# Optimization experiments

Hardware: AMD Instinct MI355X
Metric: run time of the kernel (lower is better)

Reference implementation:

```python
import jax, jax.numpy as jnp
from jax import lax
import numpy as np

RF = 1024   # receptive field
MGC = 60    # mgc feature size
UPS = 200   # upsample factor
MIX = 10    # num mixtures
FS = 256    # filter size
F = 2       # mgc frames
N = F * UPS
SQRT_HALF = 0.70710678118


def setup_inputs() -> dict:
    key = jax.random.key(0)
    ks = jax.random.split(key, 30)
    g = lambda i, shape, s=0.05: jax.random.normal(ks[i], shape, dtype=jnp.float32) * s
    return dict(
        signal=g(0, (N + RF,), 0.3),
        mgc=g(1, (F, MGC), 1.0),
        cond_w=g(2, (MGC * UPS, MGC)), cond_b=g(3, (MGC * UPS,)),
        l0_win=g(4, (FS, 1, 2)), l0_bin=g(5, (FS,)),
        l0_wg=g(6, (FS, 1, 2)), l0_bg=g(7, (FS,)),
        l0_wr=g(8, (FS, 1, 2)), l0_br=g(9, (FS,)),
        lw_in=g(10, (9, FS, FS, 2)), lb_in=g(11, (9, FS)),
        lw_g=g(12, (9, FS, FS, 2)), lb_g=g(13, (9, FS)),
        lw_r=g(14, (9, FS, FS, 2)), lb_r=g(15, (9, FS)),
        cw_in=g(16, (10, FS, MGC)), cb_in=g(17, (10, FS)),
        cw_g=g(18, (10, FS, MGC)), cb_g=g(19, (10, FS)),
        pre_w=g(20, (256, FS)), pre_b=g(21, (256,)),
        mean_w=g(22, (MIX, 256)), mean_b=g(23, (MIX,)),
        std_w=g(24, (MIX, 256)), std_b=g(25, (MIX,)),
        logit_w=g(26, (MIX, 256)), logit_b=g(27, (MIX,)),
    )


def _cond_conv(x, cond, win, bin_, wg, bg, wr, br, wci, bci, wcg, bcg):
    # x: [N, Cin, L]; cond: [N, MGC] -> out: [N, FS, L//2]
    conv = lambda w, b: lax.conv_general_dilated(
        x, w, window_strides=(2,), padding='VALID',
        dimension_numbers=('NCH', 'OIH', 'NCH')) + b[None, :, None]
    it = jnp.tanh(conv(win, bin_) + (cond @ wci.T + bci)[:, :, None])
    gt = jax.nn.sigmoid(conv(wg, bg) + (cond @ wcg.T + bcg)[:, :, None])
    return (it * gt + conv(wr, br)) * SQRT_HALF


def _forward(signal, mgc, cond_w, cond_b,
             l0_win, l0_bin, l0_wg, l0_bg, l0_wr, l0_br,
             lw_in, lb_in, lw_g, lb_g, lw_r, lb_r,
             cw_in, cb_in, cw_g, cb_g,
             pre_w, pre_b, mean_w, mean_b, std_w, std_b, logit_w, logit_b):
    n = signal.shape[0] - RF
    # sliding windows: [n, 1, RF]
    idx = jnp.arange(n)[:, None] + jnp.arange(RF)[None, :]
    x = signal[idx][:, None, :]
    # conditioning: [F, MGC] -> [F, MGC*UPS] -> [F*UPS, MGC]
    cond = jnp.tanh(mgc @ cond_w.T + cond_b).reshape(-1, MGC)
    # WaveNet stack: 10 stride-2 gated conv layers, L: 1024 -> 1
    x = _cond_conv(x, cond, l0_win, l0_bin, l0_wg, l0_bg, l0_wr, l0_br,
                   cw_in[0], cb_in[0], cw_g[0], cb_g[0])
    for i in range(9):
        x = _cond_conv(x, cond, lw_in[i], lb_in[i], lw_g[i], lb_g[i],
                       lw_r[i], lb_r[i], cw_in[i + 1], cb_in[i + 1],
                       cw_g[i + 1], cb_g[i + 1])
    pre = jax.nn.relu(x[:, :, 0] @ pre_w.T + pre_b)  # [n, 256]
    mean = pre @ mean_w.T + mean_b
    stdev = pre @ std_w.T + std_b
    logits = pre @ logit_w.T + logit_b
    return mean, stdev, logits


def reference(signal, mgc, cond_w, cond_b,
              l0_win, l0_bin, l0_wg, l0_bg, l0_wr, l0_br,
              lw_in, lb_in, lw_g, lb_g, lw_r, lb_r,
              cw_in, cb_in, cw_g, cb_g,
              pre_w, pre_b, mean_w, mean_b, std_w, std_b, logit_w, logit_b):
    return _forward(signal, mgc, cond_w, cond_b,
                    l0_win, l0_bin, l0_wg, l0_bg, l0_wr, l0_br,
                    lw_in, lb_in, lw_g, lb_g, lw_r, lb_r,
                    cw_in, cb_in, cw_g, cb_g,
                    pre_w, pre_b, mean_w, mean_b, std_w, std_b,
                    logit_w, logit_b)
```

## Files before the change

kernel.cpp:

```cpp
#include <hip/hip_runtime.h>

typedef unsigned short u16;
using bf16x8 = __attribute__((ext_vector_type(8))) short;
using f32x4  = __attribute__((ext_vector_type(4))) float;

#define SQRT_HALF 0.70710678118f

__device__ __forceinline__ u16 f2bf(float f) {
    union { float f; unsigned int i; } x; x.f = f;
    unsigned int i = x.i;
    unsigned int r = (i + 0x7FFFu + ((i >> 16) & 1u)) >> 16;
    return (u16)r;
}
__device__ __forceinline__ float bf2f(u16 u) {
    union { unsigned int i; float f; } x; x.i = ((unsigned int)u) << 16; return x.f;
}
__device__ __forceinline__ float fastrcp(float x) {
    float r; asm("v_rcp_f32 %0, %1" : "=v"(r) : "v"(x)); return r;
}
__device__ __forceinline__ float sigm(float x) {
    return fastrcp(1.0f + __expf(-x));
}
__device__ __forceinline__ float tanh_f(float x) {
    float cx = fminf(fmaxf(x, -12.f), 12.f);
    float e = __expf(2.f * cx);
    return 1.0f - 2.0f * fastrcp(e + 1.0f);
}

__device__ __forceinline__ void gld16(const u16* g, u16* l) {
    __builtin_amdgcn_global_load_lds(
        (const __attribute__((address_space(1))) void*)g,
        (__attribute__((address_space(3))) void*)l,
        16, 0, 0);
}

__global__ __launch_bounds__(256) void xpose_kernel(
        const float* __restrict__ cond_w, const float* __restrict__ cw_in,
        const float* __restrict__ cw_g,
        float* __restrict__ cond_wT, float* __restrict__ cwT_in,
        float* __restrict__ cwT_g) {
    int idx = blockIdx.x * 256 + threadIdx.x;
    if (idx < 720000) {
        int c = idx / 12000, j = idx % 12000;
        cond_wT[idx] = cond_w[(size_t)j * 60 + c];
    } else if (idx < 720000 + 153600) {
        int i = idx - 720000;
        int l = i / 15360, r = i % 15360;
        int cc = r / 256, co = r % 256;
        cwT_in[i] = cw_in[((size_t)(l * 256 + co)) * 60 + cc];
    } else if (idx < 720000 + 307200) {
        int i = idx - 720000 - 153600;
        int l = i / 15360, r = i % 15360;
        int cc = r / 256, co = r % 256;
        cwT_g[i] = cw_g[((size_t)(l * 256 + co)) * 60 + cc];
    }
}

__global__ __launch_bounds__(256) void prep_kernel(
        const float* __restrict__ mgc, const float* __restrict__ cond_wT,
        const float* __restrict__ cond_b,
        const float* __restrict__ cwT_in, const float* __restrict__ cb_in,
        const float* __restrict__ cwT_g,  const float* __restrict__ cb_g,
        const float* __restrict__ l0_bin, const float* __restrict__ lb_in,
        const float* __restrict__ l0_bg,  const float* __restrict__ lb_g,
        const float* __restrict__ lw_in, const float* __restrict__ lw_g,
        const float* __restrict__ lw_r,
        float* __restrict__ ca_in, float* __restrict__ ca_g, u16* __restrict__ Wg) {
    int b = blockIdx.x, t = threadIdx.x;
    if (b < 500) {
        __shared__ float c2[8][60];
        int l = b / 50, ng = b % 50;
        int n0 = ng * 8;
        int f = n0 / 200;
        for (int e = t; e < 480; e += 256) {
            int dn = e / 60, cc = e % 60;
            int jj = ((n0 + dn) % 200) * 60 + cc;
            float s = cond_b[jj];
            const float* mrow = mgc + f * 60;
            for (int c = 0; c < 60; ++c) s += mrow[c] * cond_wT[c * 12000 + jj];
            c2[dn][cc] = tanh_f(s);
        }
        __syncthreads();
        int co = t;
        float sib = cb_in[l * 256 + co] + (l == 0 ? l0_bin[co] : lb_in[(l - 1) * 256 + co]);
        float sgb = cb_g [l * 256 + co] + (l == 0 ? l0_bg [co] : lb_g [(l - 1) * 256 + co]);
        float si[8], sg[8];
        #pragma unroll
        for (int dn = 0; dn < 8; ++dn) { si[dn] = sib; sg[dn] = sgb; }
        const float* wiT = cwT_in + l * 15360 + co;
        const float* wgT = cwT_g  + l * 15360 + co;
        for (int cc = 0; cc < 60; ++cc) {
            float wiv = wiT[cc * 256];
            float wgv = wgT[cc * 256];
            #pragma unroll
            for (int dn = 0; dn < 8; ++dn) {
                float cv = c2[dn][cc];
                si[dn] += cv * wiv;
                sg[dn] += cv * wgv;
            }
        }
        #pragma unroll
        for (int dn = 0; dn < 8; ++dn) {
            ca_in[l * 102400 + (n0 + dn) * 256 + co] = si[dn];
            ca_g [l * 102400 + (n0 + dn) * 256 + co] = sg[dn];
        }
    } else {
        int idx = (b - 500) * 256 + t;
        if (idx < 9 * 256 * 512) {
            int kk = idx & 511;
            int co = (idx >> 9) & 255;
            int l  = idx >> 17;
            int k = kk >> 8, ci = kk & 255;
            size_t src = ((size_t)(l * 256 + co) * 256 + ci) * 2 + k;
            size_t dst = (size_t)l * 3 * 131072 + (size_t)co * 512 + kk;
            Wg[dst]              = f2bf(lw_in[src]);
            Wg[dst + 131072]     = f2bf(lw_g[src]);
            Wg[dst + 2 * 131072] = f2bf(lw_r[src]);
        }
    }
}

__global__ void l0_kernel(const float* __restrict__ signal,
                          const float* __restrict__ l0_win, const float* __restrict__ l0_wg,
                          const float* __restrict__ l0_wr,  const float* __restrict__ l0_br,
                          const float* __restrict__ ca_in0, const float* __restrict__ ca_g0,
                          u16* __restrict__ Y0, int n_start) {
    int b = blockIdx.x;
    int tg = b & 127, n_local = b >> 7;
    int n = n_start + n_local;
    int ci = threadIdx.x;
    float wi0 = l0_win[ci * 2], wi1 = l0_win[ci * 2 + 1];
    float wg0 = l0_wg [ci * 2], wg1 = l0_wg [ci * 2 + 1];
    float wr0 = l0_wr [ci * 2], wr1 = l0_wr [ci * 2 + 1];
    float cain = ca_in0[n * 256 + ci], cag = ca_g0[n * 256 + ci], br = l0_br[ci];
    for (int i = 0; i < 4; ++i) {
        int t = tg * 4 + i;
        float s0 = signal[n + 2 * t];
        float s1 = signal[n + 2 * t + 1];
        float vin = wi0 * s0 + wi1 * s1 + cain;
        float vg  = wg0 * s0 + wg1 * s1 + cag;
        float vr  = wr0 * s0 + wr1 * s1 + br;
        float o = (tanh_f(vin) * sigm(vg) + vr) * SQRT_HALF;
        Y0[((size_t)n_local * 512 + t) * 256 + ci] = f2bf(o);
    }
}

template<int BK>
__global__ __launch_bounds__(256, BK == 32 ? 3 : 2) void gemm_layer_kernel(
        const u16* __restrict__ A, const u16* __restrict__ Wg,
        const float* __restrict__ ca_in, const float* __restrict__ ca_g,
        const float* __restrict__ br, u16* __restrict__ Y,
        int M, int lg, int n_start) {
    constexpr int AC  = BK / 16;
    constexpr int BC  = (3 * BK) / 32;
    constexpr int SL  = BK / 8;
    constexpr int RSH = (BK == 32) ? 2 : 3;
    constexpr int NS  = 512 / BK;

    __shared__ __attribute__((aligned(16))) u16 A0[128 * BK];
    __shared__ __attribute__((aligned(16))) u16 A1[128 * BK];
    __shared__ __attribute__((aligned(16))) u16 B0[192 * BK];
    __shared__ __attribute__((aligned(16))) u16 B1[192 * BK];

    int mtiles = (M + 127) >> 7;
    int b = blockIdx.x;
    int mtile, cotile;
    if ((mtiles & 7) == 0) {
        int g = b >> 5, r = b & 31;
        mtile  = g * 8 + (r & 7);
        cotile = r >> 3;
    } else {
        mtile = b >> 2; cotile = b & 3;
    }
    int m0  = mtile * 128;
    int co0 = cotile * 64;
    int tid = threadIdx.x;
    int lane = tid & 63, wave = tid >> 6;
    int wm = wave & 1, wc = wave >> 1;
    int q = lane >> 4, r16 = lane & 15;

    auto swz = [](int row) { return (BK == 32) ? ((row >> 1) & 3) : (row & 7); };

    const u16* agp[AC]; unsigned aoff[AC];
    #pragma unroll
    for (int i = 0; i < AC; ++i) {
        int c = i * 256 + tid;
        int row = c >> RSH, s = c & (SL - 1);
        int m = m0 + row;
        int msafe = m < M ? m : (M - 1);
        agp[i] = A + (size_t)msafe * 512 + (s ^ swz(row)) * 8;
        aoff[i] = (unsigned)c * 8;
    }
    const u16* bgp[BC]; unsigned boff[BC];
    #pragma unroll
    for (int i = 0; i < BC; ++i) {
        int c = i * 256 + tid;
        int row = c >> RSH, s = c & (SL - 1);
        int conv = row >> 6, col = row & 63;
        bgp[i] = Wg + ((size_t)conv * 256 + co0 + col) * 512 + (s ^ swz(row)) * 8;
        boff[i] = (unsigned)c * 8;
    }

    f32x4 acc[3][4][2] = {};

    auto doIssue = [&](int ktn, u16* Al, u16* Bl) {
        #pragma unroll
        for (int i = 0; i < AC; ++i) gld16(agp[i] + ktn * BK, &Al[aoff[i]]);
        #pragma unroll
        for (int i = 0; i < BC; ++i) gld16(bgp[i] + ktn * BK, &Bl[boff[i]]);
    };
    auto doComp = [&](const u16* Al, const u16* Bl) {
        #pragma unroll
        for (int ks = 0; ks < BK / 32; ++ks) {
            bf16x8 af[4], bfr[3][2];
            #pragma unroll
            for (int ms = 0; ms < 4; ++ms) {
                int row = wm * 64 + ms * 16 + r16;
                af[ms] = *(const bf16x8*)(&Al[row * BK + (((ks * 4 + q) ^ swz(row)) * 8)]);
            }
            #pragma unroll
            for (int cv = 0; cv < 3; ++cv)
                #pragma unroll
                for (int cs = 0; cs < 2; ++cs) {
                    int row = cv * 64 + wc * 32 + cs * 16 + r16;
                    bfr[cv][cs] = *(const bf16x8*)(&Bl[row * BK + (((ks * 4 + q) ^ swz(row)) * 8)]);
                }
            __builtin_amdgcn_s_setprio(1);
            #pragma unroll
            for (int cv = 0; cv < 3; ++cv)
                #pragma unroll
                for (int ms = 0; ms < 4; ++ms)
                    #pragma unroll
                    for (int cs = 0; cs < 2; ++cs)
                        acc[cv][ms][cs] = __builtin_amdgcn_mfma_f32_16x16x32_bf16(
                            af[ms], bfr[cv][cs], acc[cv][ms][cs], 0, 0, 0);
            __builtin_amdgcn_s_setprio(0);
        }
    };
    auto waitv = []() {
        if constexpr (BK == 32)
            asm volatile("s_waitcnt vmcnt(5)\n\ts_barrier" ::: "memory");
        else
            asm volatile("s_waitcnt vmcnt(10)\n\ts_barrier" ::: "memory");
    };

    doIssue(0, A0, B0);
    doIssue(1, A1, B1);
    waitv();

    #pragma unroll
    for (int kt2 = 0; kt2 < NS / 2 - 1; ++kt2) {
        doComp(A0, B0);
        asm volatile("s_waitcnt lgkmcnt(0)\n\ts_barrier" ::: "memory");
        doIssue(2 * kt2 + 2, A0, B0);
        waitv();
        doComp(A1, B1);
        asm volatile("s_waitcnt lgkmcnt(0)\n\ts_barrier" ::: "memory");
        doIssue(2 * kt2 + 3, A1, B1);
        waitv();
    }
    doComp(A0, B0);
    asm volatile("s_waitcnt lgkmcnt(0)\n\ts_barrier" ::: "memory");
    asm volatile("s_waitcnt vmcnt(0)\n\ts_barrier" ::: "memory");
    doComp(A1, B1);

    #pragma unroll
    for (int ms = 0; ms < 4; ++ms) {
        #pragma unroll
        for (int reg = 0; reg < 4; ++reg) {
            int m = m0 + wm * 64 + ms * 16 + q * 4 + reg;
            if (m >= M) continue;
            int n = n_start + (m >> lg);
            #pragma unroll
            for (int cs = 0; cs < 2; ++cs) {
                int co = co0 + wc * 32 + cs * 16 + r16;
                float vin = acc[0][ms][cs][reg] + ca_in[n * 256 + co];
                float vg  = acc[1][ms][cs][reg] + ca_g [n * 256 + co];
                float vr  = acc[2][ms][cs][reg] + br[co];
                float o = (tanh_f(vin) * sigm(vg) + vr) * SQRT_HALF;
                Y[(size_t)m * 256 + co] = f2bf(o);
            }
        }
    }
}

__global__ __launch_bounds__(256) void head_kernel(
        const u16* __restrict__ Y9, const float* __restrict__ pre_w, const float* __restrict__ pre_b,
        const float* __restrict__ mean_w, const float* __restrict__ mean_b,
        const float* __restrict__ std_w,  const float* __restrict__ std_b,
        const float* __restrict__ logit_w, const float* __restrict__ logit_b,
        float* __restrict__ out, int n_start) {
    __shared__ float xin[256];
    __shared__ float pre[256];
    int n_local = blockIdx.x;
    int n = n_start + n_local;
    int t = threadIdx.x;
    xin[t] = bf2f(Y9[(size_t)n_local * 256 + t]);
    __syncthreads();
    float s = pre_b[t];
    const float* wrow = pre_w + (size_t)t * 256;
    for (int c = 0; c < 256; ++c) s += xin[c] * wrow[c];
    pre[t] = fmaxf(s, 0.f);
    __syncthreads();
    if (t < 30) {
        int head = t / 10, mix = t % 10;
        const float* w  = head == 0 ? mean_w : (head == 1 ? std_w : logit_w);
        const float* bb = head == 0 ? mean_b : (head == 1 ? std_b : logit_b);
        float s2 = bb[mix];
        const float* wr = w + mix * 256;
        for (int c = 0; c < 256; ++c) s2 += pre[c] * wr[c];
        out[head * 4000 + n * 10 + mix] = s2;
    }
}

extern "C" void kernel_launch(void* const* d_in, const int* in_sizes, int n_in,
                              void* d_out, int out_size, void* d_ws, size_t ws_size,
                              hipStream_t stream) {
    const float* signal  = (const float*)d_in[0];
    const float* mgc     = (const float*)d_in[1];
    const float* cond_w  = (const float*)d_in[2];
    const float* cond_b  = (const float*)d_in[3];
    const float* l0_win  = (const float*)d_in[4];
    const float* l0_bin  = (const float*)d_in[5];
    const float* l0_wg   = (const float*)d_in[6];
    const float* l0_bg   = (const float*)d_in[7];
    const float* l0_wr   = (const float*)d_in[8];
    const float* l0_br   = (const float*)d_in[9];
    const float* lw_in   = (const float*)d_in[10];
    const float* lb_in   = (const float*)d_in[11];
    const float* lw_g    = (const float*)d_in[12];
    const float* lb_g    = (const float*)d_in[13];
    const float* lw_r    = (const float*)d_in[14];
    const float* lb_r    = (const float*)d_in[15];
    const float* cw_in   = (const float*)d_in[16];
    const float* cb_in   = (const float*)d_in[17];
    const float* cw_g    = (const float*)d_in[18];
    const float* cb_g    = (const float*)d_in[19];
    const float* pre_w   = (const float*)d_in[20];
    const float* pre_b   = (const float*)d_in[21];
    const float* mean_w  = (const float*)d_in[22];
    const float* mean_b  = (const float*)d_in[23];
    const float* std_w   = (const float*)d_in[24];
    const float* std_b   = (const float*)d_in[25];
    const float* logit_w = (const float*)d_in[26];
    const float* logit_b = (const float*)d_in[27];
    float* out = (float*)d_out;

    char* p = (char*)d_ws;
    auto alloc = [&](size_t bytes) -> char* {
        char* r = p; p += (bytes + 255) & ~(size_t)255; return r;
    };
    u16*   Wg      = (u16*)alloc(7077888);
    float* ca_in   = (float*)alloc(4096000);
    float* ca_g    = (float*)alloc(4096000);
    float* cond_wT = (float*)alloc(2880000);
    float* cwT_in  = (float*)alloc(614400);
    float* cwT_g   = (float*)alloc(614400);
    size_t fixedBytes = (size_t)(p - (char*)d_ws);

    int c = 1;
    while (c < 16 && fixedBytes + (104857600ull + 52428800ull) / c + 4096 > ws_size) c <<= 1;
    u16* bufA = (u16*)alloc(104857600ull / c);
    u16* bufB = (u16*)alloc(52428800ull / c);
    int n_count = 400 / c;

    xpose_kernel<<<4013, 256, 0, stream>>>(cond_w, cw_in, cw_g, cond_wT, cwT_in, cwT_g);
    prep_kernel<<<5108, 256, 0, stream>>>(mgc, cond_wT, cond_b,
                                          cwT_in, cb_in, cwT_g, cb_g,
                                          l0_bin, lb_in, l0_bg, lb_g,
                                          lw_in, lw_g, lw_r, ca_in, ca_g, Wg);

    for (int ch = 0; ch < c; ++ch) {
        int n_start = ch * n_count;
        l0_kernel<<<n_count * 128, 256, 0, stream>>>(signal, l0_win, l0_wg, l0_wr, l0_br,
                                                     ca_in, ca_g, bufA, n_start);
        u16* src = bufA;
        u16* dst = bufB;
        for (int layer = 1; layer <= 9; ++layer) {
            int lg = 9 - layer;
            int M = n_count << lg;
            int mtiles = (M + 127) / 128;
            bool bk64 = (layer == 2) || (layer >= 5);
            if (bk64)
                gemm_layer_kernel<64><<<mtiles * 4, 256, 0, stream>>>(
                    src, Wg + (size_t)(layer - 1) * 3 * 131072,
                    ca_in + (size_t)layer * 102400, ca_g + (size_t)layer * 102400,
                    lb_r + (layer - 1) * 256, dst, M, lg, n_start);
            else
                gemm_layer_kernel<32><<<mtiles * 4, 256, 0, stream>>>(
                    src, Wg + (size_t)(layer - 1) * 3 * 131072,
                    ca_in + (size_t)layer * 102400, ca_g + (size_t)layer * 102400,
                    lb_r + (layer - 1) * 256, dst, M, lg, n_start);
            u16* tswap = src; src = dst; dst = tswap;
        }
        head_kernel<<<n_count, 256, 0, stream>>>(src, pre_w, pre_b, mean_w, mean_b,
                                                 std_w, std_b, logit_w, logit_b, out, n_start);
    }
}
```

Measured before the change: 478.0 us.

## Fuse layers 5-9 and the output head into one per-window tail kernel

Replaces the separate GEMM launches for layers 5-9 and the head kernel with one tail kernel. Each block processes two windows, keeping the shrinking activations (32->1 rows) in swizzled shared memory and running MFMA over them with weights loaded directly from global memory. This removes several small-M launches and their global round-trips of activations, at the cost of re-reading full layer weights per block with low MFMA row utilisation. It also raises the occupancy hint for the BK=32 GEMM from 3 to 4 blocks.

```diff
diff --git a/kernel.cpp b/kernel.cpp
--- a/kernel.cpp
+++ b/kernel.cpp
@@ -146,7 +146,7 @@
 }
 
 template<int BK>
-__global__ __launch_bounds__(256, BK == 32 ? 3 : 2) void gemm_layer_kernel(
+__global__ __launch_bounds__(256, BK == 32 ? 4 : 2) void gemm_layer_kernel(
         const u16* __restrict__ A, const u16* __restrict__ Wg,
         const float* __restrict__ ca_in, const float* __restrict__ ca_g,
         const float* __restrict__ br, u16* __restrict__ Y,
@@ -284,32 +284,115 @@
     }
 }
 
-__global__ __launch_bounds__(256) void head_kernel(
-        const u16* __restrict__ Y9, const float* __restrict__ pre_w, const float* __restrict__ pre_b,
+__global__ __launch_bounds__(256, 2) void tail_kernel(
+        const u16* __restrict__ Y4, const u16* __restrict__ Wg,
+        const float* __restrict__ ca_in, const float* __restrict__ ca_g,
+        const float* __restrict__ lb_r,
+        const float* __restrict__ pre_w, const float* __restrict__ pre_b,
         const float* __restrict__ mean_w, const float* __restrict__ mean_b,
         const float* __restrict__ std_w,  const float* __restrict__ std_b,
         const float* __restrict__ logit_w, const float* __restrict__ logit_b,
-        float* __restrict__ out, int n_start) {
-    __shared__ float xin[256];
-    __shared__ float pre[256];
-    int n_local = blockIdx.x;
-    int n = n_start + n_local;
-    int t = threadIdx.x;
-    xin[t] = bf2f(Y9[(size_t)n_local * 256 + t]);
+        float* __restrict__ out, int n_start, int n_end) {
+    __shared__ __attribute__((aligned(16))) u16 X[2][32][256];
+    __shared__ __attribute__((aligned(16))) u16 Yb[2][16][256];
+    __shared__ float pre[2][256];
+
+    int tid = threadIdx.x;
+    int n0 = n_start + blockIdx.x * 2;
+
+    #pragma unroll
+    for (int i = 0; i < 8; ++i) {
+        int c = i * 256 + tid;
+        int win = c >> 10, rem = c & 1023;
+        int row = rem >> 5, blk = rem & 31;
+        int n = n0 + win; if (n > n_end - 1) n = n_end - 1;
+        const u16* src = Y4 + ((size_t)(n - n_start) * 32 + row) * 256 + blk * 8;
+        *(uint4*)(&X[win][row][(blk ^ ((row >> 1) & 7)) * 8]) = *(const uint4*)src;
+    }
     __syncthreads();
-    float s = pre_b[t];
-    const float* wrow = pre_w + (size_t)t * 256;
-    for (int c = 0; c < 256; ++c) s += xin[c] * wrow[c];
-    pre[t] = fmaxf(s, 0.f);
+
+    int lane = tid & 63, w = tid >> 6;
+    int win = w & 1, cobase = (w >> 1) * 128;
+    int r16 = lane & 15, q = lane >> 4;
+    bool wvalid = (n0 + win) < n_end;
+    int n = n0 + win;
+
+    for (int l = 5; l <= 9; ++l) {
+        int Rout = 512 >> l;
+        int Rin  = Rout * 2;
+        const u16* IN = (l & 1) ? &X[win][0][0] : &Yb[win][0][0];
+        u16*      OUT = (l & 1) ? &Yb[win][0][0] : &X[win][0][0];
+        const u16* Wgl = Wg + (size_t)(l - 1) * 3 * 131072;
+        const float* cal  = ca_in + (size_t)l * 102400;
+        const float* cagl = ca_g  + (size_t)l * 102400;
+        const float* brl  = lb_r + (l - 1) * 256;
+
+        f32x4 acc[3][8] = {};
+        for (int kk = 0; kk < 16; ++kk) {
+            int row = 2 * r16 + (kk >> 3);
+            if (row >= Rin) row &= 1;
+            bf16x8 af = *(const bf16x8*)(
+                &IN[row * 256 + ((((kk & 7) * 4 + q) ^ ((row >> 1) & 7)) * 8)]);
+            bf16x8 bfr[3][8];
+            #pragma unroll
+            for (int cv = 0; cv < 3; ++cv)
+                #pragma unroll
+                for (int cf = 0; cf < 8; ++cf)
+                    bfr[cv][cf] = *(const bf16x8*)(
+                        Wgl + ((size_t)(cv * 256 + cobase + cf * 16 + r16)) * 512
+                            + kk * 32 + q * 8);
+            __builtin_amdgcn_s_setprio(1);
+            #pragma unroll
+            for (int cv = 0; cv < 3; ++cv)
+                #pragma unroll
+                for (int cf = 0; cf < 8; ++cf)
+                    acc[cv][cf] = __builtin_amdgcn_mfma_f32_16x16x32_bf16(
+                        af, bfr[cv][cf], acc[cv][cf], 0, 0, 0);
+            __builtin_amdgcn_s_setprio(0);
+        }
+
+        if (wvalid) {
+            #pragma unroll
+            for (int cf = 0; cf < 8; ++cf) {
+                int co = cobase + cf * 16 + r16;
+                #pragma unroll
+                for (int reg = 0; reg < 4; ++reg) {
+                    int tp = q * 4 + reg;
+                    if (tp < Rout) {
+                        float vin = acc[0][cf][reg] + cal [n * 256 + co];
+                        float vg  = acc[1][cf][reg] + cagl[n * 256 + co];
+                        float vr  = acc[2][cf][reg] + brl[co];
+                        float o = (tanh_f(vin) * sigm(vg) + vr) * SQRT_HALF;
+                        OUT[tp * 256 + (((co >> 3) ^ ((tp >> 1) & 7)) * 8 + (co & 7))] = f2bf(o);
+                    }
+                }
+            }
+        }
+        __syncthreads();
+    }
+
+    {
+        int t = tid;
+        for (int wn = 0; wn < 2; ++wn) {
+            if (n0 + wn >= n_end) break;
+            float s = pre_b[t];
+            const float* wrow = pre_w + (size_t)t * 256;
+            for (int c2 = 0; c2 < 256; ++c2) s += bf2f(Yb[wn][0][c2]) * wrow[c2];
+            pre[wn][t] = fmaxf(s, 0.f);
+        }
+    }
     __syncthreads();
-    if (t < 30) {
-        int head = t / 10, mix = t % 10;
-        const float* w  = head == 0 ? mean_w : (head == 1 ? std_w : logit_w);
-        const float* bb = head == 0 ? mean_b : (head == 1 ? std_b : logit_b);
-        float s2 = bb[mix];
-        const float* wr = w + mix * 256;
-        for (int c = 0; c < 256; ++c) s2 += pre[c] * wr[c];
-        out[head * 4000 + n * 10 + mix] = s2;
+    if (tid < 60) {
+        int wn = tid / 30, tt = tid % 30;
+        if (n0 + wn < n_end) {
+            int head = tt / 10, mix = tt % 10;
+            const float* wv = head == 0 ? mean_w : (head == 1 ? std_w : logit_w);
+            const float* bb = head == 0 ? mean_b : (head == 1 ? std_b : logit_b);
+            float s2 = bb[mix];
+            const float* wr = wv + mix * 256;
+            for (int c2 = 0; c2 < 256; ++c2) s2 += pre[wn][c2] * wr[c2];
+            out[head * 4000 + (n0 + wn) * 10 + mix] = s2;
+        }
     }
 }
 
@@ -376,12 +459,11 @@
                                                      ca_in, ca_g, bufA, n_start);
         u16* src = bufA;
         u16* dst = bufB;
-        for (int layer = 1; layer <= 9; ++layer) {
+        for (int layer = 1; layer <= 4; ++layer) {
             int lg = 9 - layer;
             int M = n_count << lg;
             int mtiles = (M + 127) / 128;
-            bool bk64 = (layer == 2) || (layer >= 5);
-            if (bk64)
+            if (layer == 2)
                 gemm_layer_kernel<64><<<mtiles * 4, 256, 0, stream>>>(
                     src, Wg + (size_t)(layer - 1) * 3 * 131072,
                     ca_in + (size_t)layer * 102400, ca_g + (size_t)layer * 102400,
@@ -393,7 +475,10 @@
                     lb_r + (layer - 1) * 256, dst, M, lg, n_start);
             u16* tswap = src; src = dst; dst = tswap;
         }
-        head_kernel<<<n_count, 256, 0, stream>>>(src, pre_w, pre_b, mean_w, mean_b,
-                                                 std_w, std_b, logit_w, logit_b, out, n_start);
-    }
-}
+        int nblk = (n_count + 1) / 2;
+        tail_kernel<<<nblk, 256, 0, stream>>>(src, Wg, ca_in, ca_g, lb_r,
+                                              pre_w, pre_b, mean_w, mean_b,
+                                              std_w, std_b, logit_w, logit_b,
+                                              out, n_start, n_start + n_count);
+    }
+}
```

Result: slower. 1.121 ms (+134.6%).
